# Optimization experiments

Hardware: AMD Instinct MI355X
Metric: run time of the kernel (lower is better)

The kernel has to match this reference:

```python
import jax, jax.numpy as jnp
import numpy as np

EPS = 1e-5  # torch LayerNorm default

def layer_norm(x, s, b):
    m = x.mean(-1, keepdims=True)
    v = ((x - m) ** 2).mean(-1, keepdims=True)
    return (x - m) / jnp.sqrt(v + EPS) * s + b


def setup_inputs() -> dict:
    key = jax.random.key(0)
    ks = jax.random.split(key, 24)
    N_NODES, N_EDGES = 100001, 500001   # id 0 is padding
    FEAT, TDIM = 172, 100
    B, K, G, C, L = 8192, 64, 100, 64, 2
    TOK_H, CH_H = int(0.5 * K), int(4.0 * C)

    def lin(k, fan_in, shape):
        bound = 1.0 / np.sqrt(fan_in)
        return jax.random.uniform(k, shape, jnp.float32, -bound, bound)

    inp = {}
    inp["node_table"] = jax.random.normal(ks[0], (N_NODES, FEAT), jnp.float32)
    inp["edge_table"] = jax.random.normal(ks[1], (N_EDGES, FEAT), jnp.float32)
    # TimeEncoder: fixed weights 1/10^linspace(0,9,time_dim), zero bias
    inp["time_w"] = jnp.asarray(1.0 / 10 ** np.linspace(0, 9, TDIM), jnp.float32)
    inp["proj_W"] = lin(ks[2], FEAT + TDIM, (FEAT + TDIM, C))
    inp["proj_b"] = lin(ks[3], FEAT + TDIM, (C,))
    inp["tok_ln_s"] = jnp.ones((L, K), jnp.float32)
    inp["tok_ln_b"] = jnp.zeros((L, K), jnp.float32)
    inp["tok_W1"] = lin(ks[4], K, (L, K, TOK_H))
    inp["tok_b1"] = lin(ks[5], K, (L, TOK_H))
    inp["tok_W2"] = lin(ks[6], TOK_H, (L, TOK_H, K))
    inp["tok_b2"] = lin(ks[7], TOK_H, (L, K))
    inp["ch_ln_s"] = jnp.ones((L, C), jnp.float32)
    inp["ch_ln_b"] = jnp.zeros((L, C), jnp.float32)
    inp["ch_W1"] = lin(ks[8], C, (L, C, CH_H))
    inp["ch_b1"] = lin(ks[9], C, (L, CH_H))
    inp["ch_W2"] = lin(ks[10], CH_H, (L, CH_H, C))
    inp["ch_b2"] = lin(ks[11], CH_H, (L, C))
    inp["out_W"] = lin(ks[12], C + FEAT, (C + FEAT, FEAT))
    inp["out_b"] = lin(ks[13], C + FEAT, (FEAT,))
    # precomputed neighbor-sampler outputs
    inp["node_ids"] = jax.random.randint(ks[14], (B,), 1, N_NODES)
    inp["neighbor_node_ids"] = jax.random.randint(ks[15], (B, K), 0, N_NODES)
    inp["neighbor_edge_ids"] = jax.random.randint(ks[16], (B, K), 0, N_EDGES)
    inp["gap_ids"] = jax.random.randint(ks[17], (B, G), 0, N_NODES)
    inp["node_interact_times"] = jax.random.uniform(ks[18], (B,), jnp.float32, 0.0, 1e6)
    inp["neighbor_times"] = jax.random.uniform(ks[19], (B, K), jnp.float32, 0.0, 1e6)
    return inp


def reference(node_table, edge_table, time_w, proj_W, proj_b,
              tok_ln_s, tok_ln_b, tok_W1, tok_b1, tok_W2, tok_b2,
              ch_ln_s, ch_ln_b, ch_W1, ch_b1, ch_W2, ch_b2,
              out_W, out_b,
              node_ids, neighbor_node_ids, neighbor_edge_ids, gap_ids,
              node_interact_times, neighbor_times):
    # --- gather edge features + time encoding (B, K, F+TDIM) ---
    edge_feats = edge_table[neighbor_edge_ids]                       # (B,K,F)
    dt = node_interact_times[:, None] - neighbor_times               # (B,K)
    time_feats = jnp.cos(dt[..., None] * time_w)                     # (B,K,TDIM)
    time_feats = jnp.where((neighbor_node_ids == 0)[..., None], 0.0, time_feats)
    x = jnp.concatenate([edge_feats, time_feats], axis=-1) @ proj_W + proj_b  # (B,K,C)

    # --- MLP-Mixer layers (dropout inert at eval) ---
    for l in range(tok_W1.shape[0]):
        h = layer_norm(x.transpose(0, 2, 1), tok_ln_s[l], tok_ln_b[l])      # (B,C,K)
        h = jax.nn.gelu(h @ tok_W1[l] + tok_b1[l], approximate=False)
        h = h @ tok_W2[l] + tok_b2[l]                                        # (B,C,K)
        x = h.transpose(0, 2, 1) + x                                         # token residual
        h = layer_norm(x, ch_ln_s[l], ch_ln_b[l])                            # (B,K,C)
        h = jax.nn.gelu(h @ ch_W1[l] + ch_b1[l], approximate=False)
        x = (h @ ch_W2[l] + ch_b2[l]) + x                                    # channel residual

    agg = x.mean(axis=1)                                             # (B,C)

    # --- softmax-weighted mean over time-gap neighbors ---
    node_feats = node_table[gap_ids]                                 # (B,G,F)
    valid = jnp.where(gap_ids > 0, 1.0, -1e10).astype(jnp.float32)
    scores = jax.nn.softmax(valid, axis=1)                           # (B,G)
    agg_node = (node_feats * scores[..., None]).mean(axis=1)         # (B,F)

    out = jnp.concatenate([agg, agg_node + node_table[node_ids]], axis=-1)
    return out @ out_W + out_b                                       # (B,F)
```

## Files before the change

### kernel.cpp

```cpp
#include <hip/hip_runtime.h>
#include <math.h>

#define B_    8192
#define K_    64
#define C_    64
#define FEAT_ 172
#define TDIM_ 100
#define TOKH_ 32
#define CHH_  256
#define G_    100
#define L_    2
#define CAT_  236

typedef _Float16 f16x8 __attribute__((ext_vector_type(8)));
typedef _Float16 f16x4 __attribute__((ext_vector_type(4)));
typedef float    f32x4 __attribute__((ext_vector_type(4)));

__device__ __forceinline__ float fast_cos(float p) {
    const double rev = (double)p * 0.15915494309189535;
    const double fr  = rev - __builtin_rint(rev);
#if __has_builtin(__builtin_amdgcn_cosf)
    return __builtin_amdgcn_cosf((float)fr);
#else
    return __cosf(6.283185307179586f * (float)fr);
#endif
}

__device__ __forceinline__ float gelu_f(float x) {
    const float z  = x * 0.70710678118654752f;
    const float az = fabsf(z);
    const float t  = __builtin_amdgcn_rcpf(fmaf(0.47047f, az, 1.0f));
    const float poly = t * (0.3480242f + t * (-0.0958798f + t * 0.7478556f));
    const float e  = __expf(-az * az);
    float erfv = fmaf(-poly, e, 1.0f);
    erfv = copysignf(erfv, z);
    return 0.5f * x * (1.0f + erfv);
}

__global__ __launch_bounds__(256)
void prepack_kernel(const float* __restrict__ proj_W,
                    const float* __restrict__ tW1, const float* __restrict__ tW2,
                    const float* __restrict__ cW1, const float* __restrict__ cW2,
                    const float* __restrict__ out_W,
                    _Float16* __restrict__ pW,
                    _Float16* __restrict__ pT1, _Float16* __restrict__ pT2,
                    _Float16* __restrict__ pC1, _Float16* __restrict__ pC2,
                    _Float16* __restrict__ pOW) {
    const int stride = gridDim.x * blockDim.x;
    const int t0 = blockIdx.x * blockDim.x + threadIdx.x;
    for (int i = t0; i < 64 * 288; i += stride) {
        const int c = i / 288, ii = i % 288;
        float v = 0.f;
        if (ii < 172) v = proj_W[ii * 64 + c];
        else if (ii >= 176 && ii < 276) v = proj_W[(ii - 4) * 64 + c];
        pW[i] = (_Float16)v;
    }
    for (int i = t0; i < 2 * 32 * 64; i += stride) {
        const int l = i / 2048, rem = i % 2048, j = rem / 64, k = rem % 64;
        pT1[i] = (_Float16)tW1[l * 2048 + k * 32 + j];
    }
    for (int i = t0; i < 2 * 64 * 32; i += stride) {
        const int l = i / 2048, rem = i % 2048, k = rem / 32, j = rem % 32;
        pT2[i] = (_Float16)tW2[l * 2048 + j * 64 + k];
    }
    for (int i = t0; i < 2 * 256 * 64; i += stride) {
        const int l = i / 16384, rem = i % 16384, n = rem / 64, c = rem % 64;
        pC1[i] = (_Float16)cW1[l * 16384 + c * 256 + n];
    }
    for (int i = t0; i < 2 * 64 * 256; i += stride) {
        const int l = i / 16384, rem = i % 16384, c = rem / 256, n = rem % 256;
        pC2[i] = (_Float16)cW2[l * 16384 + n * 64 + c];
    }
    for (int i = t0; i < 176 * 256; i += stride) {
        const int n = i / 256, k = i % 256;
        pOW[i] = (n < FEAT_ && k < CAT_) ? (_Float16)out_W[k * FEAT_ + n]
                                         : (_Float16)0.f;
    }
}

__global__ __launch_bounds__(256, 3)
void fused_kernel(const float* __restrict__ edge_table,
                  const float* __restrict__ time_w,
                  const _Float16* __restrict__ pW,
                  const float* __restrict__ proj_b,
                  const int*   __restrict__ nbr_nids,
                  const int*   __restrict__ nbr_eids,
                  const float* __restrict__ node_times,
                  const float* __restrict__ nbr_times,
                  const float* __restrict__ tok_ln_s, const float* __restrict__ tok_ln_b,
                  const float* __restrict__ tok_b1,   const float* __restrict__ tok_b2,
                  const float* __restrict__ ch_ln_s,  const float* __restrict__ ch_ln_b,
                  const float* __restrict__ ch_b1,    const float* __restrict__ ch_b2,
                  const _Float16* __restrict__ pT1, const _Float16* __restrict__ pT2,
                  const _Float16* __restrict__ pC1, const _Float16* __restrict__ pC2,
                  float* __restrict__ agg_out) {
    __shared__ __attribute__((aligned(16))) float    xf[2][64 * 68];
    __shared__ __attribute__((aligned(16))) _Float16 sh[2][64 * 72];

    const int bid  = blockIdx.x;
    const int t    = threadIdx.x;
    const int lane = t & 63;
    const int w    = t >> 6;
    const int r    = lane & 15;
    const int g    = lane >> 4;
    const int row16 = 16 * w + r;

    {
        const float* erow[2];
        bool  nz[2];
        float dt[2];
#pragma unroll
        for (int bb = 0; bb < 2; ++bb) {
            const size_t bgl = (size_t)(2 * bid + bb) * K_ + row16;
            erow[bb] = edge_table + (size_t)nbr_eids[bgl] * FEAT_;
            nz[bb]   = (nbr_nids[bgl] == 0);
            dt[bb]   = node_times[2 * bid + bb] - nbr_times[bgl];
        }

        f32x4 pacc[2][4];
#pragma unroll
        for (int nt = 0; nt < 4; ++nt) {
            const f32x4 pb = *(const f32x4*)&proj_b[16 * nt + 4 * g];
            pacc[0][nt] = pb; pacc[1][nt] = pb;
        }

        const int c0b = 8 * g;
#pragma unroll
        for (int kk = 0; kk < 9; ++kk) {
            const int c0 = 32 * kk + c0b;
            f16x8 af[4];
#pragma unroll
            for (int nt = 0; nt < 4; ++nt)
                af[nt] = *(const f16x8*)&pW[(16 * nt + r) * 288 + c0];
            f16x8 bf[2];
#pragma unroll
            for (int bb = 0; bb < 2; ++bb) {
                if (c0 + 8 <= FEAT_) {
                    const float4 v0 = *(const float4*)(erow[bb] + c0);
                    const float4 v1 = *(const float4*)(erow[bb] + c0 + 4);
                    bf[bb][0]=(_Float16)v0.x; bf[bb][1]=(_Float16)v0.y;
                    bf[bb][2]=(_Float16)v0.z; bf[bb][3]=(_Float16)v0.w;
                    bf[bb][4]=(_Float16)v1.x; bf[bb][5]=(_Float16)v1.y;
                    bf[bb][6]=(_Float16)v1.z; bf[bb][7]=(_Float16)v1.w;
                } else if (c0 < 176) {
                    const float4 v0 = *(const float4*)(erow[bb] + 168);
                    bf[bb][0]=(_Float16)v0.x; bf[bb][1]=(_Float16)v0.y;
                    bf[bb][2]=(_Float16)v0.z; bf[bb][3]=(_Float16)v0.w;
                    bf[bb][4]=(_Float16)0.f; bf[bb][5]=(_Float16)0.f;
                    bf[bb][6]=(_Float16)0.f; bf[bb][7]=(_Float16)0.f;
                } else {
                    const int d0 = c0 - 176;
#pragma unroll
                    for (int i = 0; i < 8; ++i) {
                        const int d = d0 + i;
                        float tv = 0.f;
                        if (d < TDIM_) tv = fast_cos(dt[bb] * time_w[d]);
                        bf[bb][i] = nz[bb] ? (_Float16)0.f : (_Float16)tv;
                    }
                }
            }
#pragma unroll
            for (int nt = 0; nt < 4; ++nt) {
                pacc[0][nt] = __builtin_amdgcn_mfma_f32_16x16x32_f16(af[nt], bf[0], pacc[0][nt], 0, 0, 0);
                pacc[1][nt] = __builtin_amdgcn_mfma_f32_16x16x32_f16(af[nt], bf[1], pacc[1][nt], 0, 0, 0);
            }
        }
#pragma unroll
        for (int bb = 0; bb < 2; ++bb)
#pragma unroll
            for (int nt = 0; nt < 4; ++nt)
                *(f32x4*)&xf[bb][row16 * 68 + 16 * nt + 4 * g] = pacc[bb][nt];
    }
    __syncthreads();

    for (int l = 0; l < L_; ++l) {
#pragma unroll
        for (int bb = 0; bb < 2; ++bb) {
            const int c0 = row16;
            float xv[16], s = 0.f, ss = 0.f;
#pragma unroll
            for (int u = 0; u < 16; ++u) {
                const float v = xf[bb][(16 * g + u) * 68 + c0];
                xv[u] = v; s += v; ss += v * v;
            }
            s += __shfl_xor(s, 16); ss += __shfl_xor(ss, 16);
            s += __shfl_xor(s, 32); ss += __shfl_xor(ss, 32);
            const float mean = s * 0.015625f;
            const float rstd = rsqrtf(ss * 0.015625f - mean * mean + 1e-5f);
            const float* tls = tok_ln_s + l * 64 + 16 * g;
            const float* tlb = tok_ln_b + l * 64 + 16 * g;
            f16x8 h0, h1;
#pragma unroll
            for (int u = 0; u < 8; ++u)
                h0[u] = (_Float16)((xv[u] - mean) * rstd * tls[u] + tlb[u]);
#pragma unroll
            for (int u = 0; u < 8; ++u)
                h1[u] = (_Float16)((xv[8 + u] - mean) * rstd * tls[8 + u] + tlb[8 + u]);
            *(f16x8*)&sh[bb][c0 * 72 + 16 * g]     = h0;
            *(f16x8*)&sh[bb][c0 * 72 + 16 * g + 8] = h1;
        }
        {
            const _Float16* W1 = pT1 + l * 2048;
            const _Float16* W2 = pT2 + l * 2048;
            f16x8 tb0[2], tb1[2];
#pragma unroll
            for (int bb = 0; bb < 2; ++bb) {
                tb0[bb] = *(const f16x8*)&sh[bb][row16 * 72 + 8 * g];
                tb1[bb] = *(const f16x8*)&sh[bb][row16 * 72 + 32 + 8 * g];
            }
#pragma unroll
            for (int nt = 0; nt < 2; ++nt) {
                const f16x8 a0 = *(const f16x8*)&W1[(16 * nt + r) * 64 + 8 * g];
                const f16x8 a1 = *(const f16x8*)&W1[(16 * nt + r) * 64 + 32 + 8 * g];
                const f32x4 bias = *(const f32x4*)&tok_b1[l * 32 + 16 * nt + 4 * g];
#pragma unroll
                for (int bb = 0; bb < 2; ++bb) {
                    f32x4 acc = bias;
                    acc = __builtin_amdgcn_mfma_f32_16x16x32_f16(a0, tb0[bb], acc, 0, 0, 0);
                    acc = __builtin_amdgcn_mfma_f32_16x16x32_f16(a1, tb1[bb], acc, 0, 0, 0);
                    f16x4 hq;
#pragma unroll
                    for (int jj = 0; jj < 4; ++jj) hq[jj] = (_Float16)gelu_f(acc[jj]);
                    *(f16x4*)&sh[bb][row16 * 72 + 16 * nt + 4 * g] = hq;
                }
            }
            f16x8 a[2];
#pragma unroll
            for (int bb = 0; bb < 2; ++bb)
                a[bb] = *(const f16x8*)&sh[bb][row16 * 72 + 8 * g];
#pragma unroll
            for (int nt = 0; nt < 4; ++nt) {
                const int kcol = 16 * nt + r;
                const float bk = tok_b2[l * 64 + kcol];
                const f16x8 bf = *(const f16x8*)&W2[kcol * 32 + 8 * g];
#pragma unroll
                for (int bb = 0; bb < 2; ++bb) {
                    f32x4 acc = {bk, bk, bk, bk};
                    acc = __builtin_amdgcn_mfma_f32_16x16x32_f16(a[bb], bf, acc, 0, 0, 0);
                    float* p = &xf[bb][kcol * 68 + 16 * w + 4 * g];
                    const f32x4 old = *(const f32x4*)p;
                    *(f32x4*)p = old + acc;
                }
            }
        }
        __syncthreads();

#pragma unroll
        for (int bb = 0; bb < 2; ++bb) {
            const int k0 = row16;
            f32x4 cv[4];
            float s = 0.f, ss = 0.f;
#pragma unroll
            for (int uu = 0; uu < 4; ++uu) {
                cv[uu] = *(const f32x4*)&xf[bb][k0 * 68 + 16 * g + 4 * uu];
#pragma unroll
                for (int e = 0; e < 4; ++e) { s += cv[uu][e]; ss += cv[uu][e] * cv[uu][e]; }
            }
            s += __shfl_xor(s, 16); ss += __shfl_xor(ss, 16);
            s += __shfl_xor(s, 32); ss += __shfl_xor(ss, 32);
            const float mean = s * 0.015625f;
            const float rstd = rsqrtf(ss * 0.015625f - mean * mean + 1e-5f);
            const float* cls = ch_ln_s + l * 64 + 16 * g;
            const float* clb = ch_ln_b + l * 64 + 16 * g;
            f16x8 h0, h1;
#pragma unroll
            for (int uu = 0; uu < 4; ++uu)
#pragma unroll
                for (int e = 0; e < 4; ++e) {
                    const float hv = (cv[uu][e] - mean) * rstd * cls[4 * uu + e] + clb[4 * uu + e];
                    if (uu < 2) h0[4 * uu + e] = (_Float16)hv;
                    else        h1[4 * (uu - 2) + e] = (_Float16)hv;
                }
            *(f16x8*)&sh[bb][k0 * 72 + 16 * g]     = h0;
            *(f16x8*)&sh[bb][k0 * 72 + 16 * g + 8] = h1;
        }
        {
            f16x8 ca0[2], ca1[2];
#pragma unroll
            for (int bb = 0; bb < 2; ++bb) {
                ca0[bb] = *(const f16x8*)&sh[bb][row16 * 72 + 8 * g];
                ca1[bb] = *(const f16x8*)&sh[bb][row16 * 72 + 32 + 8 * g];
            }
            const _Float16* Wc1 = pC1 + l * 16384;
            const _Float16* Wc2 = pC2 + l * 16384;
            f32x4 cacc[2][4];
#pragma unroll
            for (int nt = 0; nt < 4; ++nt) {
                const f32x4 cb = *(const f32x4*)&ch_b2[l * 64 + 16 * nt + 4 * g];
                cacc[0][nt] = cb; cacc[1][nt] = cb;
            }
#pragma unroll
            for (int q = 0; q < 4; ++q) {
#pragma unroll
                for (int nt = 0; nt < 4; ++nt) {
                    const int nrow = 64 * q + 16 * nt + r;
                    const f16x8 a0 = *(const f16x8*)&Wc1[nrow * 64 + 8 * g];
                    const f16x8 a1 = *(const f16x8*)&Wc1[nrow * 64 + 32 + 8 * g];
                    const f32x4 hb1 = *(const f32x4*)&ch_b1[l * 256 + 64 * q + 16 * nt + 4 * g];
#pragma unroll
                    for (int bb = 0; bb < 2; ++bb) {
                        f32x4 acc = hb1;
                        acc = __builtin_amdgcn_mfma_f32_16x16x32_f16(a0, ca0[bb], acc, 0, 0, 0);
                        acc = __builtin_amdgcn_mfma_f32_16x16x32_f16(a1, ca1[bb], acc, 0, 0, 0);
                        f16x4 hq;
#pragma unroll
                        for (int jj = 0; jj < 4; ++jj) hq[jj] = (_Float16)gelu_f(acc[jj]);
                        *(f16x4*)&sh[bb][row16 * 72 + 16 * nt + 4 * g] = hq;
                    }
                }
#pragma unroll
                for (int ks = 0; ks < 2; ++ks) {
                    f16x8 bh[2];
#pragma unroll
                    for (int bb = 0; bb < 2; ++bb)
                        bh[bb] = *(const f16x8*)&sh[bb][row16 * 72 + 32 * ks + 8 * g];
#pragma unroll
                    for (int nt2 = 0; nt2 < 4; ++nt2) {
                        const f16x8 a2 = *(const f16x8*)&Wc2[(16 * nt2 + r) * 256 + 64 * q + 32 * ks + 8 * g];
                        cacc[0][nt2] = __builtin_amdgcn_mfma_f32_16x16x32_f16(a2, bh[0], cacc[0][nt2], 0, 0, 0);
                        cacc[1][nt2] = __builtin_amdgcn_mfma_f32_16x16x32_f16(a2, bh[1], cacc[1][nt2], 0, 0, 0);
                    }
                }
            }
#pragma unroll
            for (int bb = 0; bb < 2; ++bb)
#pragma unroll
                for (int nt2 = 0; nt2 < 4; ++nt2) {
                    float* p = &xf[bb][row16 * 68 + 16 * nt2 + 4 * g];
                    const f32x4 old = *(const f32x4*)p;
                    *(f32x4*)p = old + cacc[bb][nt2];
                }
        }
        __syncthreads();
    }

#pragma unroll
    for (int bb = 0; bb < 2; ++bb) {
        float ssum = 0.f;
#pragma unroll
        for (int u = 0; u < 16; ++u) ssum += xf[bb][(16 * g + u) * 68 + row16];
        ssum += __shfl_xor(ssum, 16);
        ssum += __shfl_xor(ssum, 32);
        if (g == 0) agg_out[(size_t)(2 * bid + bb) * 64 + row16] = ssum * 0.015625f;
    }
}

__global__ __launch_bounds__(256)
void out_kernel(const float* __restrict__ node_table,
                const float* __restrict__ agg,
                const _Float16* __restrict__ pOW,
                const float* __restrict__ out_b,
                const int*   __restrict__ node_ids,
                const int*   __restrict__ gap_ids,
                float* __restrict__ out) {
    __shared__ __attribute__((aligned(16))) _Float16 inb16[16][264];
    const int t     = threadIdx.x;
    const int bbase = blockIdx.x * 16;
    const int m     = t >> 4;
    const int c16   = t & 15;
    const int b     = bbase + m;

#pragma unroll
    for (int j = 0; j < 4; ++j)
        inb16[m][c16 + 16 * j] = (_Float16)agg[(size_t)b * C_ + c16 + 16 * j];
    {
        const int c0 = 236 + c16;
        if (c0 < 264) inb16[m][c0] = (_Float16)0.f;
        const int c1 = 252 + c16;
        if (c1 < 264) inb16[m][c1] = (_Float16)0.f;
    }
    {
        const int* gid = gap_ids + (size_t)b * G_;
        float acc[11];
#pragma unroll
        for (int j = 0; j < 11; ++j) acc[j] = 0.f;
        int nv = 0;
        for (int g = 0; g < G_; ++g) {
            const int id = gid[g];
            if (id > 0) {
                ++nv;
                const float* row = node_table + (size_t)id * FEAT_;
#pragma unroll
                for (int j = 0; j < 11; ++j) {
                    const int c = c16 + 16 * j;
                    if (c < FEAT_) acc[j] += row[c];
                }
            }
        }
        const float scale = 1.0f / (float)(G_ * (nv > 0 ? nv : 1));
        const float* nrow = node_table + (size_t)node_ids[b] * FEAT_;
#pragma unroll
        for (int j = 0; j < 11; ++j) {
            const int c = c16 + 16 * j;
            if (c < FEAT_)
                inb16[m][64 + c] = (_Float16)(fmaf(acc[j], scale, nrow[c]));
        }
    }
    __syncthreads();

    const int lane = t & 63;
    const int w = t >> 6;
    const int r = lane & 15;
    const int g = lane >> 4;
    f16x8 bf[8];
#pragma unroll
    for (int kk = 0; kk < 8; ++kk)
        bf[kk] = *(const f16x8*)&inb16[r][32 * kk + 8 * g];
    for (int nt = w; nt < 11; nt += 4) {
        const int n0 = nt * 16 + 4 * g;
        const int bidx = (n0 + 4 <= FEAT_) ? n0 : (FEAT_ - 4);
        f32x4 acc = *(const f32x4*)&out_b[bidx];
#pragma unroll
        for (int kk = 0; kk < 8; ++kk) {
            const f16x8 af = *(const f16x8*)&pOW[(nt * 16 + r) * 256 + 32 * kk + 8 * g];
            acc = __builtin_amdgcn_mfma_f32_16x16x32_f16(af, bf[kk], acc, 0, 0, 0);
        }
        if (n0 + 4 <= FEAT_)
            *(f32x4*)&out[(size_t)(bbase + r) * FEAT_ + n0] = acc;
    }
}

extern "C" void kernel_launch(void* const* d_in, const int* in_sizes, int n_in,
                              void* d_out, int out_size, void* d_ws, size_t ws_size,
                              hipStream_t stream) {
    const float* node_table = (const float*)d_in[0];
    const float* edge_table = (const float*)d_in[1];
    const float* time_w     = (const float*)d_in[2];
    const float* proj_W     = (const float*)d_in[3];
    const float* proj_b     = (const float*)d_in[4];
    const float* tok_ln_s   = (const float*)d_in[5];
    const float* tok_ln_b   = (const float*)d_in[6];
    const float* tok_W1     = (const float*)d_in[7];
    const float* tok_b1     = (const float*)d_in[8];
    const float* tok_W2     = (const float*)d_in[9];
    const float* tok_b2     = (const float*)d_in[10];
    const float* ch_ln_s    = (const float*)d_in[11];
    const float* ch_ln_b    = (const float*)d_in[12];
    const float* ch_W1      = (const float*)d_in[13];
    const float* ch_b1      = (const float*)d_in[14];
    const float* ch_W2      = (const float*)d_in[15];
    const float* ch_b2      = (const float*)d_in[16];
    const float* out_W      = (const float*)d_in[17];
    const float* out_b      = (const float*)d_in[18];
    const int*   node_ids   = (const int*)d_in[19];
    const int*   nbr_nids   = (const int*)d_in[20];
    const int*   nbr_eids   = (const int*)d_in[21];
    const int*   gap_ids    = (const int*)d_in[22];
    const float* node_times = (const float*)d_in[23];
    const float* nbr_times  = (const float*)d_in[24];

    float* agg_buf = (float*)d_ws;
    _Float16* pw   = (_Float16*)(agg_buf + (size_t)B_ * C_);
    _Float16* pW   = pw;
    _Float16* pT1  = pW  + 18432;
    _Float16* pT2  = pT1 + 4096;
    _Float16* pC1  = pT2 + 4096;
    _Float16* pC2  = pC1 + 32768;
    _Float16* pOW  = pC2 + 32768;
    float* outp    = (float*)d_out;

    prepack_kernel<<<64, 256, 0, stream>>>(proj_W, tok_W1, tok_W2, ch_W1, ch_W2,
                                           out_W, pW, pT1, pT2, pC1, pC2, pOW);
    fused_kernel<<<B_ / 2, 256, 0, stream>>>(edge_table, time_w, pW, proj_b,
                                             nbr_nids, nbr_eids, node_times, nbr_times,
                                             tok_ln_s, tok_ln_b, tok_b1, tok_b2,
                                             ch_ln_s, ch_ln_b, ch_b1, ch_b2,
                                             pT1, pT2, pC1, pC2,
                                             agg_buf);
    out_kernel<<<B_ / 16, 256, 0, stream>>>(node_table, agg_buf, pOW, out_b,
                                            node_ids, gap_ids, outp);
}
```

Baseline: 540.7 us.

## Store residual stream in fp16 LDS and share one scratch buffer to raise occupancy

The per-block residual buffer moves from fp32 to fp16, and the two per-sample scratch buffers are merged into one, with the second sample's hidden activations held in registers and staged through the shared buffer one after the other. This cuts LDS per block by more than half, and the launch bound rises from 3 to 5 blocks per CU to hide the latency of gathers and MFMA work. Edge-table gathers now use nontemporal loads. The cost is that the residual is accumulated in fp16 across layers, which loses precision, and the extra register pressure needed to hit 5 blocks could cause spills.

```diff
diff --git a/kernel.cpp b/kernel.cpp
--- a/kernel.cpp
+++ b/kernel.cpp
@@ -35,6 +35,14 @@
     float erfv = fmaf(-poly, e, 1.0f);
     erfv = copysignf(erfv, z);
     return 0.5f * x * (1.0f + erfv);
+}
+
+__device__ __forceinline__ void rmw16(_Float16* p, f32x4 add) {
+    const f16x4 old = *(const f16x4*)p;
+    f16x4 nw;
+#pragma unroll
+    for (int j = 0; j < 4; ++j) nw[j] = (_Float16)((float)old[j] + add[j]);
+    *(f16x4*)p = nw;
 }
 
 __global__ __launch_bounds__(256)
@@ -78,7 +86,7 @@
     }
 }
 
-__global__ __launch_bounds__(256, 3)
+__global__ __launch_bounds__(256, 5)
 void fused_kernel(const float* __restrict__ edge_table,
                   const float* __restrict__ time_w,
                   const _Float16* __restrict__ pW,
@@ -94,8 +102,8 @@
                   const _Float16* __restrict__ pT1, const _Float16* __restrict__ pT2,
                   const _Float16* __restrict__ pC1, const _Float16* __restrict__ pC2,
                   float* __restrict__ agg_out) {
-    __shared__ __attribute__((aligned(16))) float    xf[2][64 * 68];
-    __shared__ __attribute__((aligned(16))) _Float16 sh[2][64 * 72];
+    __shared__ __attribute__((aligned(16))) _Float16 xf[2][64 * 72];
+    __shared__ __attribute__((aligned(16))) _Float16 sh[64 * 72];
 
     const int bid  = blockIdx.x;
     const int t    = threadIdx.x;
@@ -136,18 +144,14 @@
 #pragma unroll
             for (int bb = 0; bb < 2; ++bb) {
                 if (c0 + 8 <= FEAT_) {
-                    const float4 v0 = *(const float4*)(erow[bb] + c0);
-                    const float4 v1 = *(const float4*)(erow[bb] + c0 + 4);
-                    bf[bb][0]=(_Float16)v0.x; bf[bb][1]=(_Float16)v0.y;
-                    bf[bb][2]=(_Float16)v0.z; bf[bb][3]=(_Float16)v0.w;
-                    bf[bb][4]=(_Float16)v1.x; bf[bb][5]=(_Float16)v1.y;
-                    bf[bb][6]=(_Float16)v1.z; bf[bb][7]=(_Float16)v1.w;
+                    const f32x4 v0 = __builtin_nontemporal_load((const f32x4*)(erow[bb] + c0));
+                    const f32x4 v1 = __builtin_nontemporal_load((const f32x4*)(erow[bb] + c0 + 4));
+#pragma unroll
+                    for (int j = 0; j < 4; ++j) { bf[bb][j] = (_Float16)v0[j]; bf[bb][4 + j] = (_Float16)v1[j]; }
                 } else if (c0 < 176) {
-                    const float4 v0 = *(const float4*)(erow[bb] + 168);
-                    bf[bb][0]=(_Float16)v0.x; bf[bb][1]=(_Float16)v0.y;
-                    bf[bb][2]=(_Float16)v0.z; bf[bb][3]=(_Float16)v0.w;
-                    bf[bb][4]=(_Float16)0.f; bf[bb][5]=(_Float16)0.f;
-                    bf[bb][6]=(_Float16)0.f; bf[bb][7]=(_Float16)0.f;
+                    const f32x4 v0 = __builtin_nontemporal_load((const f32x4*)(erow[bb] + 168));
+#pragma unroll
+                    for (int j = 0; j < 4; ++j) { bf[bb][j] = (_Float16)v0[j]; bf[bb][4 + j] = (_Float16)0.f; }
                 } else {
                     const int d0 = c0 - 176;
 #pragma unroll
@@ -168,19 +172,24 @@
 #pragma unroll
         for (int bb = 0; bb < 2; ++bb)
 #pragma unroll
-            for (int nt = 0; nt < 4; ++nt)
-                *(f32x4*)&xf[bb][row16 * 68 + 16 * nt + 4 * g] = pacc[bb][nt];
+            for (int nt = 0; nt < 4; ++nt) {
+                f16x4 st;
+#pragma unroll
+                for (int j = 0; j < 4; ++j) st[j] = (_Float16)pacc[bb][nt][j];
+                *(f16x4*)&xf[bb][row16 * 72 + 16 * nt + 4 * g] = st;
+            }
     }
     __syncthreads();
 
     for (int l = 0; l < L_; ++l) {
+        f16x8 tb0[2], tb1[2];
 #pragma unroll
         for (int bb = 0; bb < 2; ++bb) {
             const int c0 = row16;
             float xv[16], s = 0.f, ss = 0.f;
 #pragma unroll
             for (int u = 0; u < 16; ++u) {
-                const float v = xf[bb][(16 * g + u) * 68 + c0];
+                const float v = (float)xf[bb][(16 * g + u) * 72 + c0];
                 xv[u] = v; s += v; ss += v * v;
             }
             s += __shfl_xor(s, 16); ss += __shfl_xor(ss, 16);
@@ -196,38 +205,41 @@
 #pragma unroll
             for (int u = 0; u < 8; ++u)
                 h1[u] = (_Float16)((xv[8 + u] - mean) * rstd * tls[8 + u] + tlb[8 + u]);
-            *(f16x8*)&sh[bb][c0 * 72 + 16 * g]     = h0;
-            *(f16x8*)&sh[bb][c0 * 72 + 16 * g + 8] = h1;
+            *(f16x8*)&sh[c0 * 72 + 16 * g]     = h0;
+            *(f16x8*)&sh[c0 * 72 + 16 * g + 8] = h1;
+            tb0[bb] = *(const f16x8*)&sh[row16 * 72 + 8 * g];
+            tb1[bb] = *(const f16x8*)&sh[row16 * 72 + 32 + 8 * g];
         }
         {
             const _Float16* W1 = pT1 + l * 2048;
             const _Float16* W2 = pT2 + l * 2048;
-            f16x8 tb0[2], tb1[2];
-#pragma unroll
-            for (int bb = 0; bb < 2; ++bb) {
-                tb0[bb] = *(const f16x8*)&sh[bb][row16 * 72 + 8 * g];
-                tb1[bb] = *(const f16x8*)&sh[bb][row16 * 72 + 32 + 8 * g];
-            }
+            f32x4 h1save[2];
+            f16x8 a[2];
 #pragma unroll
             for (int nt = 0; nt < 2; ++nt) {
                 const f16x8 a0 = *(const f16x8*)&W1[(16 * nt + r) * 64 + 8 * g];
                 const f16x8 a1 = *(const f16x8*)&W1[(16 * nt + r) * 64 + 32 + 8 * g];
                 const f32x4 bias = *(const f32x4*)&tok_b1[l * 32 + 16 * nt + 4 * g];
-#pragma unroll
-                for (int bb = 0; bb < 2; ++bb) {
-                    f32x4 acc = bias;
-                    acc = __builtin_amdgcn_mfma_f32_16x16x32_f16(a0, tb0[bb], acc, 0, 0, 0);
-                    acc = __builtin_amdgcn_mfma_f32_16x16x32_f16(a1, tb1[bb], acc, 0, 0, 0);
-                    f16x4 hq;
-#pragma unroll
-                    for (int jj = 0; jj < 4; ++jj) hq[jj] = (_Float16)gelu_f(acc[jj]);
-                    *(f16x4*)&sh[bb][row16 * 72 + 16 * nt + 4 * g] = hq;
-                }
-            }
-            f16x8 a[2];
-#pragma unroll
-            for (int bb = 0; bb < 2; ++bb)
-                a[bb] = *(const f16x8*)&sh[bb][row16 * 72 + 8 * g];
+                f32x4 acc0 = bias, acc1 = bias;
+                acc0 = __builtin_amdgcn_mfma_f32_16x16x32_f16(a0, tb0[0], acc0, 0, 0, 0);
+                acc0 = __builtin_amdgcn_mfma_f32_16x16x32_f16(a1, tb1[0], acc0, 0, 0, 0);
+                acc1 = __builtin_amdgcn_mfma_f32_16x16x32_f16(a0, tb0[1], acc1, 0, 0, 0);
+                acc1 = __builtin_amdgcn_mfma_f32_16x16x32_f16(a1, tb1[1], acc1, 0, 0, 0);
+                f16x4 hq;
+#pragma unroll
+                for (int jj = 0; jj < 4; ++jj) hq[jj] = (_Float16)gelu_f(acc0[jj]);
+                *(f16x4*)&sh[row16 * 72 + 16 * nt + 4 * g] = hq;
+                h1save[nt] = acc1;
+            }
+            a[0] = *(const f16x8*)&sh[row16 * 72 + 8 * g];
+#pragma unroll
+            for (int nt = 0; nt < 2; ++nt) {
+                f16x4 hq;
+#pragma unroll
+                for (int jj = 0; jj < 4; ++jj) hq[jj] = (_Float16)gelu_f(h1save[nt][jj]);
+                *(f16x4*)&sh[row16 * 72 + 16 * nt + 4 * g] = hq;
+            }
+            a[1] = *(const f16x8*)&sh[row16 * 72 + 8 * g];
 #pragma unroll
             for (int nt = 0; nt < 4; ++nt) {
                 const int kcol = 16 * nt + r;
@@ -237,25 +249,23 @@
                 for (int bb = 0; bb < 2; ++bb) {
                     f32x4 acc = {bk, bk, bk, bk};
                     acc = __builtin_amdgcn_mfma_f32_16x16x32_f16(a[bb], bf, acc, 0, 0, 0);
-                    float* p = &xf[bb][kcol * 68 + 16 * w + 4 * g];
-                    const f32x4 old = *(const f32x4*)p;
-                    *(f32x4*)p = old + acc;
+                    rmw16(&xf[bb][kcol * 72 + 16 * w + 4 * g], acc);
                 }
             }
         }
         __syncthreads();
 
+        f16x8 ca0[2], ca1[2];
 #pragma unroll
         for (int bb = 0; bb < 2; ++bb) {
             const int k0 = row16;
-            f32x4 cv[4];
-            float s = 0.f, ss = 0.f;
-#pragma unroll
-            for (int uu = 0; uu < 4; ++uu) {
-                cv[uu] = *(const f32x4*)&xf[bb][k0 * 68 + 16 * g + 4 * uu];
-#pragma unroll
-                for (int e = 0; e < 4; ++e) { s += cv[uu][e]; ss += cv[uu][e] * cv[uu][e]; }
-            }
+            const f16x8 cva = *(const f16x8*)&xf[bb][k0 * 72 + 16 * g];
+            const f16x8 cvb = *(const f16x8*)&xf[bb][k0 * 72 + 16 * g + 8];
+            float cv[16], s = 0.f, ss = 0.f;
+#pragma unroll
+            for (int e = 0; e < 8; ++e) { cv[e] = (float)cva[e]; cv[8 + e] = (float)cvb[e]; }
+#pragma unroll
+            for (int e = 0; e < 16; ++e) { s += cv[e]; ss += cv[e] * cv[e]; }
             s += __shfl_xor(s, 16); ss += __shfl_xor(ss, 16);
             s += __shfl_xor(s, 32); ss += __shfl_xor(ss, 32);
             const float mean = s * 0.015625f;
@@ -264,23 +274,16 @@
             const float* clb = ch_ln_b + l * 64 + 16 * g;
             f16x8 h0, h1;
 #pragma unroll
-            for (int uu = 0; uu < 4; ++uu)
-#pragma unroll
-                for (int e = 0; e < 4; ++e) {
-                    const float hv = (cv[uu][e] - mean) * rstd * cls[4 * uu + e] + clb[4 * uu + e];
-                    if (uu < 2) h0[4 * uu + e] = (_Float16)hv;
-                    else        h1[4 * (uu - 2) + e] = (_Float16)hv;
-                }
-            *(f16x8*)&sh[bb][k0 * 72 + 16 * g]     = h0;
-            *(f16x8*)&sh[bb][k0 * 72 + 16 * g + 8] = h1;
+            for (int e = 0; e < 8; ++e) {
+                h0[e] = (_Float16)((cv[e] - mean) * rstd * cls[e] + clb[e]);
+                h1[e] = (_Float16)((cv[8 + e] - mean) * rstd * cls[8 + e] + clb[8 + e]);
+            }
+            *(f16x8*)&sh[k0 * 72 + 16 * g]     = h0;
+            *(f16x8*)&sh[k0 * 72 + 16 * g + 8] = h1;
+            ca0[bb] = *(const f16x8*)&sh[row16 * 72 + 8 * g];
+            ca1[bb] = *(const f16x8*)&sh[row16 * 72 + 32 + 8 * g];
         }
         {
-            f16x8 ca0[2], ca1[2];
-#pragma unroll
-            for (int bb = 0; bb < 2; ++bb) {
-                ca0[bb] = *(const f16x8*)&sh[bb][row16 * 72 + 8 * g];
-                ca1[bb] = *(const f16x8*)&sh[bb][row16 * 72 + 32 + 8 * g];
-            }
             const _Float16* Wc1 = pC1 + l * 16384;
             const _Float16* Wc2 = pC2 + l * 16384;
             f32x4 cacc[2][4];
@@ -291,45 +294,50 @@
             }
 #pragma unroll
             for (int q = 0; q < 4; ++q) {
+                f32x4 h1save[4];
 #pragma unroll
                 for (int nt = 0; nt < 4; ++nt) {
                     const int nrow = 64 * q + 16 * nt + r;
                     const f16x8 a0 = *(const f16x8*)&Wc1[nrow * 64 + 8 * g];
                     const f16x8 a1 = *(const f16x8*)&Wc1[nrow * 64 + 32 + 8 * g];
                     const f32x4 hb1 = *(const f32x4*)&ch_b1[l * 256 + 64 * q + 16 * nt + 4 * g];
-#pragma unroll
-                    for (int bb = 0; bb < 2; ++bb) {
-                        f32x4 acc = hb1;
-                        acc = __builtin_amdgcn_mfma_f32_16x16x32_f16(a0, ca0[bb], acc, 0, 0, 0);
-                        acc = __builtin_amdgcn_mfma_f32_16x16x32_f16(a1, ca1[bb], acc, 0, 0, 0);
-                        f16x4 hq;
-#pragma unroll
-                        for (int jj = 0; jj < 4; ++jj) hq[jj] = (_Float16)gelu_f(acc[jj]);
-                        *(f16x4*)&sh[bb][row16 * 72 + 16 * nt + 4 * g] = hq;
-                    }
+                    f32x4 acc0 = hb1, acc1 = hb1;
+                    acc0 = __builtin_amdgcn_mfma_f32_16x16x32_f16(a0, ca0[0], acc0, 0, 0, 0);
+                    acc0 = __builtin_amdgcn_mfma_f32_16x16x32_f16(a1, ca1[0], acc0, 0, 0, 0);
+                    acc1 = __builtin_amdgcn_mfma_f32_16x16x32_f16(a0, ca0[1], acc1, 0, 0, 0);
+                    acc1 = __builtin_amdgcn_mfma_f32_16x16x32_f16(a1, ca1[1], acc1, 0, 0, 0);
+                    f16x4 hq;
+#pragma unroll
+                    for (int jj = 0; jj < 4; ++jj) hq[jj] = (_Float16)gelu_f(acc0[jj]);
+                    *(f16x4*)&sh[row16 * 72 + 16 * nt + 4 * g] = hq;
+                    h1save[nt] = acc1;
                 }
-#pragma unroll
-                for (int ks = 0; ks < 2; ++ks) {
-                    f16x8 bh[2];
-#pragma unroll
-                    for (int bb = 0; bb < 2; ++bb)
-                        bh[bb] = *(const f16x8*)&sh[bb][row16 * 72 + 32 * ks + 8 * g];
+                f16x8 bh0[2], bh1[2];
+                bh0[0] = *(const f16x8*)&sh[row16 * 72 + 8 * g];
+                bh0[1] = *(const f16x8*)&sh[row16 * 72 + 32 + 8 * g];
+#pragma unroll
+                for (int nt = 0; nt < 4; ++nt) {
+                    f16x4 hq;
+#pragma unroll
+                    for (int jj = 0; jj < 4; ++jj) hq[jj] = (_Float16)gelu_f(h1save[nt][jj]);
+                    *(f16x4*)&sh[row16 * 72 + 16 * nt + 4 * g] = hq;
+                }
+                bh1[0] = *(const f16x8*)&sh[row16 * 72 + 8 * g];
+                bh1[1] = *(const f16x8*)&sh[row16 * 72 + 32 + 8 * g];
+#pragma unroll
+                for (int ks = 0; ks < 2; ++ks)
 #pragma unroll
                     for (int nt2 = 0; nt2 < 4; ++nt2) {
                         const f16x8 a2 = *(const f16x8*)&Wc2[(16 * nt2 + r) * 256 + 64 * q + 32 * ks + 8 * g];
-                        cacc[0][nt2] = __builtin_amdgcn_mfma_f32_16x16x32_f16(a2, bh[0], cacc[0][nt2], 0, 0, 0);
-                        cacc[1][nt2] = __builtin_amdgcn_mfma_f32_16x16x32_f16(a2, bh[1], cacc[1][nt2], 0, 0, 0);
+                        cacc[0][nt2] = __builtin_amdgcn_mfma_f32_16x16x32_f16(a2, bh0[ks], cacc[0][nt2], 0, 0, 0);
+                        cacc[1][nt2] = __builtin_amdgcn_mfma_f32_16x16x32_f16(a2, bh1[ks], cacc[1][nt2], 0, 0, 0);
                     }
-                }
             }
 #pragma unroll
             for (int bb = 0; bb < 2; ++bb)
 #pragma unroll
-                for (int nt2 = 0; nt2 < 4; ++nt2) {
-                    float* p = &xf[bb][row16 * 68 + 16 * nt2 + 4 * g];
-                    const f32x4 old = *(const f32x4*)p;
-                    *(f32x4*)p = old + cacc[bb][nt2];
-                }
+                for (int nt2 = 0; nt2 < 4; ++nt2)
+                    rmw16(&xf[bb][row16 * 72 + 16 * nt2 + 4 * g], cacc[bb][nt2]);
         }
         __syncthreads();
     }
@@ -338,7 +346,7 @@
     for (int bb = 0; bb < 2; ++bb) {
         float ssum = 0.f;
 #pragma unroll
-        for (int u = 0; u < 16; ++u) ssum += xf[bb][(16 * g + u) * 68 + row16];
+        for (int u = 0; u < 16; ++u) ssum += (float)xf[bb][(16 * g + u) * 72 + row16];
         ssum += __shfl_xor(ssum, 16);
         ssum += __shfl_xor(ssum, 32);
         if (g == 0) agg_out[(size_t)(2 * bid + bb) * 64 + row16] = ssum * 0.015625f;
```

Result: slower. 716.2 us (+32.5%).

## Double-buffer weight fragment loads across projection and channel-MLP MFMA loops

Applied to the files above, without the earlier changes.

Prefetches the next k-step of projection weights into a second register buffer so global loads overlap the current MFMAs. The channel MLP is restructured into eight half-steps, each with double-buffered W1/W2 fragments, interleaving the GELU hidden-tile write with the W2 accumulation. Token-MLP weights are hoisted to the top of each layer, and edge-table reads use nontemporal loads. The extra buffers raise register pressure, which may lower occupancy.

```diff
diff --git a/kernel.cpp b/kernel.cpp
--- a/kernel.cpp
+++ b/kernel.cpp
@@ -125,29 +125,32 @@
         }
 
         const int c0b = 8 * g;
+        f16x8 af[2][4];
+#pragma unroll
+        for (int nt = 0; nt < 4; ++nt)
+            af[0][nt] = *(const f16x8*)&pW[(16 * nt + r) * 288 + c0b];
 #pragma unroll
         for (int kk = 0; kk < 9; ++kk) {
+            const int cur = kk & 1;
+            if (kk < 8) {
+                const int c1 = 32 * (kk + 1) + c0b;
+#pragma unroll
+                for (int nt = 0; nt < 4; ++nt)
+                    af[cur ^ 1][nt] = *(const f16x8*)&pW[(16 * nt + r) * 288 + c1];
+            }
             const int c0 = 32 * kk + c0b;
-            f16x8 af[4];
-#pragma unroll
-            for (int nt = 0; nt < 4; ++nt)
-                af[nt] = *(const f16x8*)&pW[(16 * nt + r) * 288 + c0];
             f16x8 bf[2];
 #pragma unroll
             for (int bb = 0; bb < 2; ++bb) {
                 if (c0 + 8 <= FEAT_) {
-                    const float4 v0 = *(const float4*)(erow[bb] + c0);
-                    const float4 v1 = *(const float4*)(erow[bb] + c0 + 4);
-                    bf[bb][0]=(_Float16)v0.x; bf[bb][1]=(_Float16)v0.y;
-                    bf[bb][2]=(_Float16)v0.z; bf[bb][3]=(_Float16)v0.w;
-                    bf[bb][4]=(_Float16)v1.x; bf[bb][5]=(_Float16)v1.y;
-                    bf[bb][6]=(_Float16)v1.z; bf[bb][7]=(_Float16)v1.w;
+                    const f32x4 v0 = __builtin_nontemporal_load((const f32x4*)(erow[bb] + c0));
+                    const f32x4 v1 = __builtin_nontemporal_load((const f32x4*)(erow[bb] + c0 + 4));
+#pragma unroll
+                    for (int j = 0; j < 4; ++j) { bf[bb][j] = (_Float16)v0[j]; bf[bb][4 + j] = (_Float16)v1[j]; }
                 } else if (c0 < 176) {
-                    const float4 v0 = *(const float4*)(erow[bb] + 168);
-                    bf[bb][0]=(_Float16)v0.x; bf[bb][1]=(_Float16)v0.y;
-                    bf[bb][2]=(_Float16)v0.z; bf[bb][3]=(_Float16)v0.w;
-                    bf[bb][4]=(_Float16)0.f; bf[bb][5]=(_Float16)0.f;
-                    bf[bb][6]=(_Float16)0.f; bf[bb][7]=(_Float16)0.f;
+                    const f32x4 v0 = __builtin_nontemporal_load((const f32x4*)(erow[bb] + 168));
+#pragma unroll
+                    for (int j = 0; j < 4; ++j) { bf[bb][j] = (_Float16)v0[j]; bf[bb][4 + j] = (_Float16)0.f; }
                 } else {
                     const int d0 = c0 - 176;
 #pragma unroll
@@ -161,8 +164,8 @@
             }
 #pragma unroll
             for (int nt = 0; nt < 4; ++nt) {
-                pacc[0][nt] = __builtin_amdgcn_mfma_f32_16x16x32_f16(af[nt], bf[0], pacc[0][nt], 0, 0, 0);
-                pacc[1][nt] = __builtin_amdgcn_mfma_f32_16x16x32_f16(af[nt], bf[1], pacc[1][nt], 0, 0, 0);
+                pacc[0][nt] = __builtin_amdgcn_mfma_f32_16x16x32_f16(af[cur][nt], bf[0], pacc[0][nt], 0, 0, 0);
+                pacc[1][nt] = __builtin_amdgcn_mfma_f32_16x16x32_f16(af[cur][nt], bf[1], pacc[1][nt], 0, 0, 0);
             }
         }
 #pragma unroll
@@ -174,6 +177,18 @@
     __syncthreads();
 
     for (int l = 0; l < L_; ++l) {
+        const _Float16* W1 = pT1 + l * 2048;
+        const _Float16* W2 = pT2 + l * 2048;
+        f16x8 ta0[2], ta1[2], wg2[4];
+#pragma unroll
+        for (int nt = 0; nt < 2; ++nt) {
+            ta0[nt] = *(const f16x8*)&W1[(16 * nt + r) * 64 + 8 * g];
+            ta1[nt] = *(const f16x8*)&W1[(16 * nt + r) * 64 + 32 + 8 * g];
+        }
+#pragma unroll
+        for (int nt = 0; nt < 4; ++nt)
+            wg2[nt] = *(const f16x8*)&W2[(16 * nt + r) * 32 + 8 * g];
+
 #pragma unroll
         for (int bb = 0; bb < 2; ++bb) {
             const int c0 = row16;
@@ -200,8 +215,6 @@
             *(f16x8*)&sh[bb][c0 * 72 + 16 * g + 8] = h1;
         }
         {
-            const _Float16* W1 = pT1 + l * 2048;
-            const _Float16* W2 = pT2 + l * 2048;
             f16x8 tb0[2], tb1[2];
 #pragma unroll
             for (int bb = 0; bb < 2; ++bb) {
@@ -210,14 +223,12 @@
             }
 #pragma unroll
             for (int nt = 0; nt < 2; ++nt) {
-                const f16x8 a0 = *(const f16x8*)&W1[(16 * nt + r) * 64 + 8 * g];
-                const f16x8 a1 = *(const f16x8*)&W1[(16 * nt + r) * 64 + 32 + 8 * g];
                 const f32x4 bias = *(const f32x4*)&tok_b1[l * 32 + 16 * nt + 4 * g];
 #pragma unroll
                 for (int bb = 0; bb < 2; ++bb) {
                     f32x4 acc = bias;
-                    acc = __builtin_amdgcn_mfma_f32_16x16x32_f16(a0, tb0[bb], acc, 0, 0, 0);
-                    acc = __builtin_amdgcn_mfma_f32_16x16x32_f16(a1, tb1[bb], acc, 0, 0, 0);
+                    acc = __builtin_amdgcn_mfma_f32_16x16x32_f16(ta0[nt], tb0[bb], acc, 0, 0, 0);
+                    acc = __builtin_amdgcn_mfma_f32_16x16x32_f16(ta1[nt], tb1[bb], acc, 0, 0, 0);
                     f16x4 hq;
 #pragma unroll
                     for (int jj = 0; jj < 4; ++jj) hq[jj] = (_Float16)gelu_f(acc[jj]);
@@ -232,11 +243,10 @@
             for (int nt = 0; nt < 4; ++nt) {
                 const int kcol = 16 * nt + r;
                 const float bk = tok_b2[l * 64 + kcol];
-                const f16x8 bf = *(const f16x8*)&W2[kcol * 32 + 8 * g];
 #pragma unroll
                 for (int bb = 0; bb < 2; ++bb) {
                     f32x4 acc = {bk, bk, bk, bk};
-                    acc = __builtin_amdgcn_mfma_f32_16x16x32_f16(a[bb], bf, acc, 0, 0, 0);
+                    acc = __builtin_amdgcn_mfma_f32_16x16x32_f16(a[bb], wg2[nt], acc, 0, 0, 0);
                     float* p = &xf[bb][kcol * 68 + 16 * w + 4 * g];
                     const f32x4 old = *(const f32x4*)p;
                     *(f32x4*)p = old + acc;
@@ -289,37 +299,57 @@
                 const f32x4 cb = *(const f32x4*)&ch_b2[l * 64 + 16 * nt + 4 * g];
                 cacc[0][nt] = cb; cacc[1][nt] = cb;
             }
-#pragma unroll
-            for (int q = 0; q < 4; ++q) {
-#pragma unroll
-                for (int nt = 0; nt < 4; ++nt) {
-                    const int nrow = 64 * q + 16 * nt + r;
-                    const f16x8 a0 = *(const f16x8*)&Wc1[nrow * 64 + 8 * g];
-                    const f16x8 a1 = *(const f16x8*)&Wc1[nrow * 64 + 32 + 8 * g];
-                    const f32x4 hb1 = *(const f32x4*)&ch_b1[l * 256 + 64 * q + 16 * nt + 4 * g];
-#pragma unroll
-                    for (int bb = 0; bb < 2; ++bb) {
-                        f32x4 acc = hb1;
-                        acc = __builtin_amdgcn_mfma_f32_16x16x32_f16(a0, ca0[bb], acc, 0, 0, 0);
-                        acc = __builtin_amdgcn_mfma_f32_16x16x32_f16(a1, ca1[bb], acc, 0, 0, 0);
-                        f16x4 hq;
-#pragma unroll
-                        for (int jj = 0; jj < 4; ++jj) hq[jj] = (_Float16)gelu_f(acc[jj]);
-                        *(f16x4*)&sh[bb][row16 * 72 + 16 * nt + 4 * g] = hq;
+            f16x8 w1a[2][2], w1b[2][2], w2f[2][4];
+#pragma unroll
+            for (int u = 0; u < 2; ++u) {
+                const int nrow = 16 * u + r;
+                w1a[0][u] = *(const f16x8*)&Wc1[nrow * 64 + 8 * g];
+                w1b[0][u] = *(const f16x8*)&Wc1[nrow * 64 + 32 + 8 * g];
+            }
+#pragma unroll
+            for (int u = 0; u < 4; ++u)
+                w2f[0][u] = *(const f16x8*)&Wc2[(16 * u + r) * 256 + 8 * g];
+
+#pragma unroll
+            for (int h = 0; h < 8; ++h) {
+                const int cur = h & 1, nxt = cur ^ 1;
+                const int q = h >> 1, half = h & 1;
+                if (h < 7) {
+                    const int q2 = (h + 1) >> 1, half2 = (h + 1) & 1;
+#pragma unroll
+                    for (int u = 0; u < 2; ++u) {
+                        const int nrow = 64 * q2 + 16 * (2 * half2 + u) + r;
+                        w1a[nxt][u] = *(const f16x8*)&Wc1[nrow * 64 + 8 * g];
+                        w1b[nxt][u] = *(const f16x8*)&Wc1[nrow * 64 + 32 + 8 * g];
                     }
-                }
-#pragma unroll
-                for (int ks = 0; ks < 2; ++ks) {
-                    f16x8 bh[2];
-#pragma unroll
-                    for (int bb = 0; bb < 2; ++bb)
-                        bh[bb] = *(const f16x8*)&sh[bb][row16 * 72 + 32 * ks + 8 * g];
-#pragma unroll
-                    for (int nt2 = 0; nt2 < 4; ++nt2) {
-                        const f16x8 a2 = *(const f16x8*)&Wc2[(16 * nt2 + r) * 256 + 64 * q + 32 * ks + 8 * g];
-                        cacc[0][nt2] = __builtin_amdgcn_mfma_f32_16x16x32_f16(a2, bh[0], cacc[0][nt2], 0, 0, 0);
-                        cacc[1][nt2] = __builtin_amdgcn_mfma_f32_16x16x32_f16(a2, bh[1], cacc[1][nt2], 0, 0, 0);
+#pragma unroll
+                    for (int u = 0; u < 4; ++u)
+                        w2f[nxt][u] = *(const f16x8*)&Wc2[(16 * u + r) * 256 + 64 * q2 + 32 * half2 + 8 * g];
+                }
+#pragma unroll
+                for (int u = 0; u < 2; ++u) {
+                    const int ntab = 2 * half + u;
+                    const f32x4 hb1 = *(const f32x4*)&ch_b1[l * 256 + 64 * q + 16 * ntab + 4 * g];
+                    f32x4 acc0 = hb1, acc1 = hb1;
+                    acc0 = __builtin_amdgcn_mfma_f32_16x16x32_f16(w1a[cur][u], ca0[0], acc0, 0, 0, 0);
+                    acc0 = __builtin_amdgcn_mfma_f32_16x16x32_f16(w1b[cur][u], ca1[0], acc0, 0, 0, 0);
+                    acc1 = __builtin_amdgcn_mfma_f32_16x16x32_f16(w1a[cur][u], ca0[1], acc1, 0, 0, 0);
+                    acc1 = __builtin_amdgcn_mfma_f32_16x16x32_f16(w1b[cur][u], ca1[1], acc1, 0, 0, 0);
+                    f16x4 hq0, hq1;
+#pragma unroll
+                    for (int jj = 0; jj < 4; ++jj) {
+                        hq0[jj] = (_Float16)gelu_f(acc0[jj]);
+                        hq1[jj] = (_Float16)gelu_f(acc1[jj]);
                     }
+                    *(f16x4*)&sh[0][row16 * 72 + 16 * ntab + 4 * g] = hq0;
+                    *(f16x4*)&sh[1][row16 * 72 + 16 * ntab + 4 * g] = hq1;
+                }
+                const f16x8 bh0 = *(const f16x8*)&sh[0][row16 * 72 + 32 * half + 8 * g];
+                const f16x8 bh1 = *(const f16x8*)&sh[1][row16 * 72 + 32 * half + 8 * g];
+#pragma unroll
+                for (int nt2 = 0; nt2 < 4; ++nt2) {
+                    cacc[0][nt2] = __builtin_amdgcn_mfma_f32_16x16x32_f16(w2f[cur][nt2], bh0, cacc[0][nt2], 0, 0, 0);
+                    cacc[1][nt2] = __builtin_amdgcn_mfma_f32_16x16x32_f16(w2f[cur][nt2], bh1, cacc[1][nt2], 0, 0, 0);
                 }
             }
 #pragma unroll
```

New measurement: 621.0 us. +14.8%, slower.
